# Kernel optimization log

Measured on AMD Instinct MI355X. Metric: run time of the kernel, lower is better.

## Reference

```python
import jax, jax.numpy as jnp
import numpy as np

# tiny-cuda-nn HashGrid config from the module
N_LEVELS = 12
F_PER_LEVEL = 2
LOG2_T = 16
T = 1 << LOG2_T            # 65536 entries per level
BASE_RES = 4
PER_LEVEL_SCALE = 1.61
HASH_PRIME_Y = np.uint32(2654435761)
HIDDEN = 256
OUT = 3
N_POINTS = 1048576

# per-level scale / resolution (tcnn: scale = base*s^l - 1, res = ceil(scale)+1)
_LEVEL_SCALES = [BASE_RES * (PER_LEVEL_SCALE ** l) - 1.0 for l in range(N_LEVELS)]
_LEVEL_RES = [int(np.ceil(s)) + 1 for s in _LEVEL_SCALES]

_CORNERS = np.array([[0, 0], [1, 0], [0, 1], [1, 1]], dtype=np.uint32)  # [4,2]


def hash_encode(x, tables):
    """x: [N,2] in [0,1); tables: [L,T,F]. Returns [N, L*F]."""
    offs_u = jnp.asarray(_CORNERS)                      # [4,2] uint32
    offs_f = offs_u.astype(x.dtype)                     # [4,2]
    feats = []
    for l in range(N_LEVELS):
        s = _LEVEL_SCALES[l]
        res = _LEVEL_RES[l]
        pos = x * jnp.asarray(s, x.dtype) + 0.5         # [N,2]
        p0f = jnp.floor(pos)
        w = pos - p0f                                   # [N,2] frac, differentiable
        p0 = p0f.astype(jnp.uint32)                     # [N,2]
        c = p0[:, None, :] + offs_u[None]               # [N,4,2] corner coords
        # bilinear weight per corner: prod over dims of (w if offset==1 else 1-w)
        wc = jnp.where(offs_f[None] == 1.0, w[:, None, :], 1.0 - w[:, None, :]).prod(-1)  # [N,4]
        if res * res <= T:
            # dense (tight grid) indexing
            cx = jnp.minimum(c[..., 0], np.uint32(res - 1))
            cy = jnp.minimum(c[..., 1], np.uint32(res - 1))
            idx = cx + cy * np.uint32(res)
        else:
            # spatial hash: x*1 XOR y*prime, masked to table size
            idx = (c[..., 0] ^ (c[..., 1] * HASH_PRIME_Y)) & np.uint32(T - 1)
        f = tables[l][idx.astype(jnp.int32)]            # [N,4,F] gather
        feats.append((wc[..., None] * f).sum(axis=1))   # [N,F]
    return jnp.concatenate(feats, axis=-1)              # [N, L*F]


def setup_inputs() -> dict:
    key = jax.random.key(0)
    ks = jax.random.split(key, 10)
    x = jax.random.uniform(ks[0], (N_POINTS, 2), dtype=jnp.float32)
    # tcnn initializes hash tables uniform in [-1e-4, 1e-4]
    tables = jax.random.uniform(ks[1], (N_LEVELS, T, F_PER_LEVEL), dtype=jnp.float32,
                                minval=-1e-4, maxval=1e-4)
    d_in = N_LEVELS * F_PER_LEVEL

    def lin(k, fan_in, fan_out):
        bound = 1.0 / np.sqrt(fan_in)
        kw, kb = jax.random.split(k)
        W = jax.random.uniform(kw, (fan_in, fan_out), dtype=jnp.float32, minval=-bound, maxval=bound)
        b = jax.random.uniform(kb, (fan_out,), dtype=jnp.float32, minval=-bound, maxval=bound)
        return W, b

    W1, b1 = lin(ks[2], d_in, HIDDEN)
    W2, b2 = lin(ks[3], HIDDEN, HIDDEN)
    W3, b3 = lin(ks[4], HIDDEN, HIDDEN)
    Wo, bo = lin(ks[5], HIDDEN, OUT)
    return {"x": x, "tables": tables, "W1": W1, "b1": b1, "W2": W2, "b2": b2,
            "W3": W3, "b3": b3, "Wo": Wo, "bo": bo}


def reference(x, tables, W1, b1, W2, b2, W3, b3, Wo, bo):
    enc = hash_encode(x, tables)                        # [N,24]
    h = jax.nn.relu(enc @ W1 + b1)
    h = jax.nn.relu(h @ W2 + b2)
    h = jax.nn.relu(h @ W3 + b3)
    return h @ Wo + bo                                  # [N,3]
```

## Files before the change

kernel.cpp:

```cpp
#include <hip/hip_runtime.h>

typedef _Float16 f16;
typedef _Float16 f16x2 __attribute__((ext_vector_type(2)));
typedef _Float16 f16x4 __attribute__((ext_vector_type(4)));
typedef _Float16 f16x8 __attribute__((ext_vector_type(8)));
typedef float    f32x4 __attribute__((ext_vector_type(4)));

#define ES 40
#define NPTS 128

static __device__ const float c_scale[12] = {
  3.0f, 5.44f, 9.3684f, 15.693124f, 25.87592964f, 42.2702467204f,
  68.665097219844f, 111.16080652394884f, 179.5788985035576f,
  289.7320265907278f, 467.0785628110717f, 752.6064861258255f };
static __device__ const unsigned c_res[12] = {4,7,11,17,27,44,70,113,181,291,469,754};

__device__ __forceinline__ f16x4 relu_pk(f32x4 v) {
  f16x2 lo = __builtin_bit_cast(f16x2,
      __builtin_amdgcn_cvt_pkrtz(fmaxf(v[0], 0.0f), fmaxf(v[1], 0.0f)));
  f16x2 hi = __builtin_bit_cast(f16x2,
      __builtin_amdgcn_cvt_pkrtz(fmaxf(v[2], 0.0f), fmaxf(v[3], 0.0f)));
  f16x4 r; r[0] = lo[0]; r[1] = lo[1]; r[2] = hi[0]; r[3] = hi[1];
  return r;
}

__global__ __launch_bounds__(256) void prep_weights(
    const float* __restrict__ W1, const float* __restrict__ W2,
    const float* __restrict__ W3, const float* __restrict__ Wo,
    f16* __restrict__ ws)
{
  int i = blockIdx.x * 256 + threadIdx.x;
  if (i < 8192) {
    int o = i >> 5, k = i & 31;
    ws[i] = (k < 24) ? (f16)W1[k * 256 + o] : (f16)0.0f;
  } else if (i < 73728) {
    int j = i - 8192; int o = j >> 8, k = j & 255;
    ws[i] = (f16)W2[k * 256 + o];
  } else if (i < 139264) {
    int j = i - 73728; int o = j >> 8, k = j & 255;
    ws[i] = (f16)W3[k * 256 + o];
  } else if (i < 143360) {
    int j = i - 139264; int o = j >> 8, k = j & 255;
    ws[i] = (o < 3) ? (f16)Wo[k * 3 + o] : (f16)0.0f;
  }
}

__device__ __forceinline__ f16x2 enc_level_dense(
    float2 xy, float s, unsigned res, const float* __restrict__ tbl)
{
  float px = __fadd_rn(__fmul_rn(xy.x, s), 0.5f);
  float py = __fadd_rn(__fmul_rn(xy.y, s), 0.5f);
  float fx = floorf(px), fy = floorf(py);
  float wx = px - fx, wy = py - fy;
  unsigned ix = (unsigned)fx, iy = (unsigned)fy;
  unsigned rm = res - 1u;
  unsigned x0 = min(ix, rm);
  unsigned y0 = min(iy, rm), y1 = min(iy + 1u, rm);
  bool xe = (ix >= rm);
  f32x4 r0 = *(const f32x4*)(tbl + (x0 + y0 * res) * 2);
  f32x4 r1 = *(const f32x4*)(tbl + (x0 + y1 * res) * 2);
  float f00x = r0[0], f00y = r0[1];
  float f10x = xe ? r0[0] : r0[2], f10y = xe ? r0[1] : r0[3];
  float f01x = r1[0], f01y = r1[1];
  float f11x = xe ? r1[0] : r1[2], f11y = xe ? r1[1] : r1[3];
  float w00 = (1.f - wx) * (1.f - wy), w10 = wx * (1.f - wy);
  float w01 = (1.f - wx) * wy,         w11 = wx * wy;
  float e0 = w00 * f00x + w10 * f10x + w01 * f01x + w11 * f11x;
  float e1 = w00 * f00y + w10 * f10y + w01 * f01y + w11 * f11y;
  f16x2 pk; pk[0] = (f16)e0; pk[1] = (f16)e1;
  return pk;
}

__device__ __forceinline__ f16x2 enc_level_hash(
    float2 xy, float s, const float* __restrict__ tbl)
{
  float px = __fadd_rn(__fmul_rn(xy.x, s), 0.5f);
  float py = __fadd_rn(__fmul_rn(xy.y, s), 0.5f);
  float fx = floorf(px), fy = floorf(py);
  float wx = px - fx, wy = py - fy;
  unsigned ix = (unsigned)fx, iy = (unsigned)fy;
  unsigned h0 = iy * 2654435761u, h1 = (iy + 1u) * 2654435761u;
  unsigned i00 = (ix ^ h0) & 65535u,  i10 = ((ix + 1u) ^ h0) & 65535u;
  unsigned i01 = (ix ^ h1) & 65535u,  i11 = ((ix + 1u) ^ h1) & 65535u;
  const float2* tb = (const float2*)tbl;
  float2 f00 = tb[i00], f10 = tb[i10], f01 = tb[i01], f11 = tb[i11];
  float w00 = (1.f - wx) * (1.f - wy), w10 = wx * (1.f - wy);
  float w01 = (1.f - wx) * wy,         w11 = wx * wy;
  float e0 = w00 * f00.x + w10 * f10.x + w01 * f01.x + w11 * f11.x;
  float e1 = w00 * f00.y + w10 * f10.y + w01 * f01.y + w11 * f11.y;
  f16x2 pk; pk[0] = (f16)e0; pk[1] = (f16)e1;
  return pk;
}

template<bool NEXT_OUT>
__device__ __forceinline__ void layer256_pipe(
    f16* __restrict__ h, const f16* __restrict__ WT,
    const f32x4* bv, f16x8* cur0, f16x8* cur1,
    const f16* __restrict__ WTn, const float* __restrict__ bn,
    f16x8* nxt0, f16x8* nxt1, f32x4* bvn, f16x8* aout,
    const int* vbase, const int* wbase, int w, int l15, int g)
{
  f32x4 acc[4][8];
  #pragma unroll
  for (int mt = 0; mt < 4; ++mt)
    #pragma unroll
    for (int nt = 0; nt < 8; ++nt) acc[mt][nt] = bv[mt];

  f16x8 abuf[3][4];
  #pragma unroll
  for (int mt = 0; mt < 4; ++mt) { abuf[0][mt] = cur0[mt]; abuf[1][mt] = cur1[mt]; }

  const char* hb = (const char*)h;
  #pragma unroll
  for (int ks = 0; ks < 8; ++ks) {
    if (ks < 6) {
      #pragma unroll
      for (int mt = 0; mt < 4; ++mt)
        abuf[(ks+2)%3][mt] = *(const f16x8*)(WT + (w*64 + mt*16 + l15)*256 + (ks+2)*32 + g*8);
    } else if (ks == 6) {
      if (NEXT_OUT) {
        #pragma unroll
        for (int q = 0; q < 4; ++q)
          aout[q] = *(const f16x8*)(WTn + l15*256 + q*32 + g*8);
      } else {
        #pragma unroll
        for (int mt = 0; mt < 4; ++mt)
          nxt0[mt] = *(const f16x8*)(WTn + (w*64 + mt*16 + l15)*256 + g*8);
        #pragma unroll
        for (int mt = 0; mt < 4; ++mt)
          bvn[mt] = *(const f32x4*)(bn + w*64 + mt*16 + g*4);
      }
    } else {
      if (NEXT_OUT) {
        #pragma unroll
        for (int q = 0; q < 4; ++q)
          aout[4+q] = *(const f16x8*)(WTn + l15*256 + (4+q)*32 + g*8);
      } else {
        #pragma unroll
        for (int mt = 0; mt < 4; ++mt)
          nxt1[mt] = *(const f16x8*)(WTn + (w*64 + mt*16 + l15)*256 + 32 + g*8);
      }
    }
    #pragma unroll
    for (int nt = 0; nt < 8; ++nt) {
      f16x8 b = *(const f16x8*)(hb + vbase[ks] + nt*8192);
      #pragma unroll
      for (int mt = 0; mt < 4; ++mt)
        acc[mt][nt] = __builtin_amdgcn_mfma_f32_16x16x32_f16(abuf[ks%3][mt], b, acc[mt][nt], 0, 0, 0);
    }
  }
  __syncthreads();
  #pragma unroll
  for (int mt = 0; mt < 4; ++mt) {
    #pragma unroll
    for (int nt = 0; nt < 8; ++nt) {
      f16x4 hv = relu_pk(acc[mt][nt]);
      *(f16x4*)((char*)h + wbase[mt] + nt*8192) = hv;
    }
  }
  __syncthreads();
}

__global__ __launch_bounds__(256, 2) void hashmlp_kernel(
    const float* __restrict__ x, const float* __restrict__ tables,
    const float* __restrict__ b1, const float* __restrict__ b2,
    const float* __restrict__ b3, const float* __restrict__ bo,
    const f16* __restrict__ ws, float* __restrict__ out)
{
  __shared__ __align__(16) f16 s_enc[NPTS * ES];
  __shared__ __align__(16) f16 s_h[NPTS * 256];

  const int tid = threadIdx.x;
  const int blk = blockIdx.x;
  const int w = tid >> 6, lane = tid & 63;
  const int l15 = lane & 15, g = lane >> 4;

  const f16* W1T = ws;
  const f16* W2T = ws + 8192;
  const f16* W3T = ws + 73728;
  const f16* WoT = ws + 139264;

  f16x8 a1[4], pn0[4], pn1[4];
  f32x4 bvA[4], bvB[4];
  #pragma unroll
  for (int mt = 0; mt < 4; ++mt) {
    a1[mt]  = *(const f16x8*)(W1T + (w*64 + mt*16 + l15)*32 + g*8);
    pn0[mt] = *(const f16x8*)(W2T + (w*64 + mt*16 + l15)*256 + g*8);
    pn1[mt] = *(const f16x8*)(W2T + (w*64 + mt*16 + l15)*256 + 32 + g*8);
    bvA[mt] = *(const f32x4*)(b1 + w*64 + mt*16 + g*4);
    bvB[mt] = *(const f32x4*)(b2 + w*64 + mt*16 + g*4);
  }
  float bo0 = bo[0], bo1 = bo[1], bo2 = bo[2];

  int vbase[8], wbase[4];
  {
    int K = (l15 & 7) << 4;
    #pragma unroll
    for (int ks = 0; ks < 8; ++ks)
      vbase[ks] = l15*512 + ((ks*64 + g*16) ^ K);
    #pragma unroll
    for (int mt = 0; mt < 4; ++mt)
      wbase[mt] = l15*512 + (((w*64 + mt*16 + g*4)*2) ^ K);
  }

  {
    int p = tid >> 1, sub = tid & 1;
    int gp = blk * NPTS + p;
    float2 xy = ((const float2*)x)[gp];
    #pragma unroll
    for (int j = 0; j < 5; ++j) {
      int l = j * 2 + sub;
      f16x2 pk = enc_level_dense(xy, c_scale[l], c_res[l], tables + l * 131072);
      *(f16x2*)(&s_enc[p * ES + l * 2]) = pk;
    }
    {
      int l = 10 + sub;
      f16x2 pk = enc_level_hash(xy, c_scale[l], tables + l * 131072);
      *(f16x2*)(&s_enc[p * ES + l * 2]) = pk;
    }
    f16x4 z; z[0] = (f16)0.0f; z[1] = (f16)0.0f; z[2] = (f16)0.0f; z[3] = (f16)0.0f;
    *(f16x4*)(&s_enc[p * ES + 24 + sub * 4]) = z;
  }
  __syncthreads();

  {
    f32x4 acc[4][8];
    #pragma unroll
    for (int mt = 0; mt < 4; ++mt)
      #pragma unroll
      for (int nt = 0; nt < 8; ++nt) acc[mt][nt] = bvA[mt];
    #pragma unroll
    for (int nt = 0; nt < 8; ++nt) {
      f16x8 b = *(const f16x8*)(&s_enc[(nt*16 + l15) * ES + g*8]);
      #pragma unroll
      for (int mt = 0; mt < 4; ++mt)
        acc[mt][nt] = __builtin_amdgcn_mfma_f32_16x16x32_f16(a1[mt], b, acc[mt][nt], 0, 0, 0);
    }
    #pragma unroll
    for (int mt = 0; mt < 4; ++mt) {
      #pragma unroll
      for (int nt = 0; nt < 8; ++nt) {
        f16x4 hv = relu_pk(acc[mt][nt]);
        *(f16x4*)((char*)s_h + wbase[mt] + nt*8192) = hv;
      }
    }
  }
  __syncthreads();

  f16x8 qn0[4], qn1[4], aout[8];
  f32x4 bvC[4];
  layer256_pipe<false>(s_h, W2T, bvB, pn0, pn1, W3T, b3, qn0, qn1, bvC, aout,
                       vbase, wbase, w, l15, g);
  layer256_pipe<true >(s_h, W3T, bvC, qn0, qn1, WoT, nullptr, pn0, pn1, bvC, aout,
                       vbase, wbase, w, l15, g);

  {
    f32x4 acc0 = (f32x4)0.0f, acc1 = (f32x4)0.0f;
    const char* hb = (const char*)s_h;
    #pragma unroll
    for (int ks = 0; ks < 8; ++ks) {
      f16x8 b0 = *(const f16x8*)(hb + vbase[ks] + (2*w+0)*8192);
      f16x8 b1v = *(const f16x8*)(hb + vbase[ks] + (2*w+1)*8192);
      acc0 = __builtin_amdgcn_mfma_f32_16x16x32_f16(aout[ks], b0, acc0, 0, 0, 0);
      acc1 = __builtin_amdgcn_mfma_f32_16x16x32_f16(aout[ks], b1v, acc1, 0, 0, 0);
    }
    if (g == 0) {
      int gp0 = blk * NPTS + (2*w+0) * 16 + l15;
      int gp1 = blk * NPTS + (2*w+1) * 16 + l15;
      out[gp0 * 3 + 0] = acc0[0] + bo0;
      out[gp0 * 3 + 1] = acc0[1] + bo1;
      out[gp0 * 3 + 2] = acc0[2] + bo2;
      out[gp1 * 3 + 0] = acc1[0] + bo0;
      out[gp1 * 3 + 1] = acc1[1] + bo1;
      out[gp1 * 3 + 2] = acc1[2] + bo2;
    }
  }
}

extern "C" void kernel_launch(void* const* d_in, const int* in_sizes, int n_in,
                              void* d_out, int out_size, void* d_ws, size_t ws_size,
                              hipStream_t stream) {
  const float* x  = (const float*)d_in[0];
  const float* tb = (const float*)d_in[1];
  const float* W1 = (const float*)d_in[2];
  const float* b1 = (const float*)d_in[3];
  const float* W2 = (const float*)d_in[4];
  const float* b2 = (const float*)d_in[5];
  const float* W3 = (const float*)d_in[6];
  const float* b3 = (const float*)d_in[7];
  const float* Wo = (const float*)d_in[8];
  const float* bo = (const float*)d_in[9];
  f16* ws = (f16*)d_ws;

  prep_weights<<<560, 256, 0, stream>>>(W1, W2, W3, Wo, ws);
  hashmlp_kernel<<<8192, 256, 0, stream>>>(x, tb, b1, b2, b3, bo, ws, (float*)d_out);
}
```

Baseline: 362.1 us.

## Split 256-wide layers into point halves to overlap epilogue with MFMA

Each hidden layer is split into two halves over points (64 each), with separate accumulators. The ReLU/store epilogue of one half is interleaved with the MFMA loop of the other half, and the output layer is split the same way. This replaces the per-layer sync-epilogue-sync pattern with a staggered schedule meant to overlap LDS writes with matrix math. It holds two accumulator sets, which may raise register pressure under the 2-blocks-per-CU launch bound, and it reloads the A-operand weights once per half.

```diff
diff --git a/kernel.cpp b/kernel.cpp
--- a/kernel.cpp
+++ b/kernel.cpp
@@ -8,6 +8,7 @@
 
 #define ES 40
 #define NPTS 128
+#define HALF_B 32768
 
 static __device__ const float c_scale[12] = {
   3.0f, 5.44f, 9.3684f, 15.693124f, 25.87592964f, 42.2702467204f,
@@ -92,25 +93,23 @@
   return pk;
 }
 
-template<bool NEXT_OUT>
-__device__ __forceinline__ void layer256_pipe(
-    f16* __restrict__ h, const f16* __restrict__ WT,
-    const f32x4* bv, f16x8* cur0, f16x8* cur1,
+template<int TAILKIND>
+__device__ __forceinline__ void mfma_half(
+    const char* hb, int halfbase, const f16* __restrict__ WT,
+    const f32x4* bv, const f16x8* cur0, const f16x8* cur1,
     const f16* __restrict__ WTn, const float* __restrict__ bn,
     f16x8* nxt0, f16x8* nxt1, f32x4* bvn, f16x8* aout,
-    const int* vbase, const int* wbase, int w, int l15, int g)
-{
-  f32x4 acc[4][8];
+    const int* vbase, int w, int l15, int g, f32x4 (&acc)[4][4])
+{
   #pragma unroll
   for (int mt = 0; mt < 4; ++mt)
     #pragma unroll
-    for (int nt = 0; nt < 8; ++nt) acc[mt][nt] = bv[mt];
+    for (int nt = 0; nt < 4; ++nt) acc[mt][nt] = bv[mt];
 
   f16x8 abuf[3][4];
   #pragma unroll
   for (int mt = 0; mt < 4; ++mt) { abuf[0][mt] = cur0[mt]; abuf[1][mt] = cur1[mt]; }
 
-  const char* hb = (const char*)h;
   #pragma unroll
   for (int ks = 0; ks < 8; ++ks) {
     if (ks < 6) {
@@ -118,47 +117,51 @@
       for (int mt = 0; mt < 4; ++mt)
         abuf[(ks+2)%3][mt] = *(const f16x8*)(WT + (w*64 + mt*16 + l15)*256 + (ks+2)*32 + g*8);
     } else if (ks == 6) {
-      if (NEXT_OUT) {
+      if constexpr (TAILKIND == 1 || TAILKIND == 2) {
+        #pragma unroll
+        for (int mt = 0; mt < 4; ++mt)
+          nxt0[mt] = *(const f16x8*)(WTn + (w*64 + mt*16 + l15)*256 + g*8);
+        if constexpr (TAILKIND == 2) {
+          #pragma unroll
+          for (int mt = 0; mt < 4; ++mt)
+            bvn[mt] = *(const f32x4*)(bn + w*64 + mt*16 + g*4);
+        }
+      } else if constexpr (TAILKIND == 3) {
         #pragma unroll
         for (int q = 0; q < 4; ++q)
           aout[q] = *(const f16x8*)(WTn + l15*256 + q*32 + g*8);
-      } else {
+      }
+    } else {
+      if constexpr (TAILKIND == 1 || TAILKIND == 2) {
         #pragma unroll
         for (int mt = 0; mt < 4; ++mt)
-          nxt0[mt] = *(const f16x8*)(WTn + (w*64 + mt*16 + l15)*256 + g*8);
-        #pragma unroll
-        for (int mt = 0; mt < 4; ++mt)
-          bvn[mt] = *(const f32x4*)(bn + w*64 + mt*16 + g*4);
-      }
-    } else {
-      if (NEXT_OUT) {
+          nxt1[mt] = *(const f16x8*)(WTn + (w*64 + mt*16 + l15)*256 + 32 + g*8);
+      } else if constexpr (TAILKIND == 3) {
         #pragma unroll
         for (int q = 0; q < 4; ++q)
           aout[4+q] = *(const f16x8*)(WTn + l15*256 + (4+q)*32 + g*8);
-      } else {
-        #pragma unroll
-        for (int mt = 0; mt < 4; ++mt)
-          nxt1[mt] = *(const f16x8*)(WTn + (w*64 + mt*16 + l15)*256 + 32 + g*8);
       }
     }
     #pragma unroll
-    for (int nt = 0; nt < 8; ++nt) {
-      f16x8 b = *(const f16x8*)(hb + vbase[ks] + nt*8192);
+    for (int nt = 0; nt < 4; ++nt) {
+      f16x8 b = *(const f16x8*)(hb + vbase[ks] + halfbase + nt*8192);
       #pragma unroll
       for (int mt = 0; mt < 4; ++mt)
         acc[mt][nt] = __builtin_amdgcn_mfma_f32_16x16x32_f16(abuf[ks%3][mt], b, acc[mt][nt], 0, 0, 0);
     }
   }
-  __syncthreads();
-  #pragma unroll
-  for (int mt = 0; mt < 4; ++mt) {
-    #pragma unroll
-    for (int nt = 0; nt < 8; ++nt) {
+}
+
+__device__ __forceinline__ void epi_half(
+    char* hb, int halfbase, const f32x4 (&acc)[4][4], const int* wbase)
+{
+  #pragma unroll
+  for (int mt = 0; mt < 4; ++mt)
+    #pragma unroll
+    for (int nt = 0; nt < 4; ++nt) {
       f16x4 hv = relu_pk(acc[mt][nt]);
-      *(f16x4*)((char*)h + wbase[mt] + nt*8192) = hv;
-    }
-  }
-  __syncthreads();
+      *(f16x4*)(hb + wbase[mt] + halfbase + nt*8192) = hv;
+    }
 }
 
 __global__ __launch_bounds__(256, 2) void hashmlp_kernel(
@@ -223,6 +226,8 @@
   }
   __syncthreads();
 
+  char* hb = (char*)s_h;
+
   {
     f32x4 acc[4][8];
     #pragma unroll
@@ -237,43 +242,62 @@
         acc[mt][nt] = __builtin_amdgcn_mfma_f32_16x16x32_f16(a1[mt], b, acc[mt][nt], 0, 0, 0);
     }
     #pragma unroll
-    for (int mt = 0; mt < 4; ++mt) {
+    for (int mt = 0; mt < 4; ++mt)
       #pragma unroll
       for (int nt = 0; nt < 8; ++nt) {
         f16x4 hv = relu_pk(acc[mt][nt]);
-        *(f16x4*)((char*)s_h + wbase[mt] + nt*8192) = hv;
+        *(f16x4*)(hb + wbase[mt] + nt*8192) = hv;
       }
-    }
-  }
-  __syncthreads();
-
+  }
+  __syncthreads();
+
+  f32x4 accA[4][4], accB[4][4];
   f16x8 qn0[4], qn1[4], aout[8];
   f32x4 bvC[4];
-  layer256_pipe<false>(s_h, W2T, bvB, pn0, pn1, W3T, b3, qn0, qn1, bvC, aout,
-                       vbase, wbase, w, l15, g);
-  layer256_pipe<true >(s_h, W3T, bvC, qn0, qn1, WoT, nullptr, pn0, pn1, bvC, aout,
-                       vbase, wbase, w, l15, g);
-
-  {
-    f32x4 acc0 = (f32x4)0.0f, acc1 = (f32x4)0.0f;
-    const char* hb = (const char*)s_h;
-    #pragma unroll
-    for (int ks = 0; ks < 8; ++ks) {
-      f16x8 b0 = *(const f16x8*)(hb + vbase[ks] + (2*w+0)*8192);
-      f16x8 b1v = *(const f16x8*)(hb + vbase[ks] + (2*w+1)*8192);
-      acc0 = __builtin_amdgcn_mfma_f32_16x16x32_f16(aout[ks], b0, acc0, 0, 0, 0);
-      acc1 = __builtin_amdgcn_mfma_f32_16x16x32_f16(aout[ks], b1v, acc1, 0, 0, 0);
-    }
-    if (g == 0) {
-      int gp0 = blk * NPTS + (2*w+0) * 16 + l15;
-      int gp1 = blk * NPTS + (2*w+1) * 16 + l15;
-      out[gp0 * 3 + 0] = acc0[0] + bo0;
-      out[gp0 * 3 + 1] = acc0[1] + bo1;
-      out[gp0 * 3 + 2] = acc0[2] + bo2;
-      out[gp1 * 3 + 0] = acc1[0] + bo0;
-      out[gp1 * 3 + 1] = acc1[1] + bo1;
-      out[gp1 * 3 + 2] = acc1[2] + bo2;
-    }
+
+  mfma_half<1>(hb, 0, W2T, bvB, pn0, pn1, W2T, nullptr, qn0, qn1, nullptr, nullptr,
+               vbase, w, l15, g, accA);
+  __syncthreads();
+
+  epi_half(hb, 0, accA, wbase);
+  mfma_half<2>(hb, HALF_B, W2T, bvB, qn0, qn1, W3T, b3, pn0, pn1, bvC, nullptr,
+               vbase, w, l15, g, accB);
+  __syncthreads();
+
+  epi_half(hb, HALF_B, accB, wbase);
+  mfma_half<1>(hb, 0, W3T, bvC, pn0, pn1, W3T, nullptr, qn0, qn1, nullptr, nullptr,
+               vbase, w, l15, g, accA);
+  __syncthreads();
+
+  epi_half(hb, 0, accA, wbase);
+  mfma_half<3>(hb, HALF_B, W3T, bvC, qn0, qn1, WoT, nullptr, nullptr, nullptr, nullptr, aout,
+               vbase, w, l15, g, accB);
+  __syncthreads();
+
+  epi_half(hb, HALF_B, accB, wbase);
+  f32x4 accO0 = (f32x4)0.0f;
+  #pragma unroll
+  for (int ks = 0; ks < 8; ++ks) {
+    f16x8 b0 = *(const f16x8*)(hb + vbase[ks] + w*8192);
+    accO0 = __builtin_amdgcn_mfma_f32_16x16x32_f16(aout[ks], b0, accO0, 0, 0, 0);
+  }
+  __syncthreads();
+
+  f32x4 accO1 = (f32x4)0.0f;
+  #pragma unroll
+  for (int ks = 0; ks < 8; ++ks) {
+    f16x8 b1v = *(const f16x8*)(hb + vbase[ks] + HALF_B + w*8192);
+    accO1 = __builtin_amdgcn_mfma_f32_16x16x32_f16(aout[ks], b1v, accO1, 0, 0, 0);
+  }
+  if (g == 0) {
+    int gp0 = blk * NPTS + w * 16 + l15;
+    int gp1 = blk * NPTS + 64 + w * 16 + l15;
+    out[gp0 * 3 + 0] = accO0[0] + bo0;
+    out[gp0 * 3 + 1] = accO0[1] + bo1;
+    out[gp0 * 3 + 2] = accO0[2] + bo2;
+    out[gp1 * 3 + 0] = accO1[0] + bo0;
+    out[gp1 * 3 + 1] = accO1[1] + bo1;
+    out[gp1 * 3 + 2] = accO1[2] + bo2;
   }
 }
 
```

Measured after the change: 549.4 us. 51.7% more time.
